# Performance work log

Measured on AMD Instinct MI355X. Metric: run time of the kernel, lower is better.

Reference implementation:

```python
import jax, jax.numpy as jnp
import numpy as np

G_NUM, K_DEG = 3, 3  # grid intervals, spline order (module defaults)
LN_EPS = 1e-5


def _bspline_basis(x, grid, k):
    """Cox-de Boor B-spline basis. x: [N, D], grid: [D, G+2k+1] -> [N, D, G+k]."""
    xg = x[:, :, None]                      # [N, D, 1]
    g = grid[None, :, :]                    # [1, D, M]
    B = ((xg >= g[..., :-1]) & (xg < g[..., 1:])).astype(x.dtype)  # degree 0
    for d in range(1, k + 1):
        left = (xg - g[..., :-(d + 1)]) / (g[..., d:-1] - g[..., :-(d + 1)])
        right = (g[..., d + 1:] - xg) / (g[..., d + 1:] - g[..., 1:-d])
        B = left * B[..., :-1] + right * B[..., 1:]
    return B                                # [N, D, G+k]


def _kan_layer(x, grid, coef, scale_base, scale_sp, node_scale, node_bias):
    # spline branch: fold per-edge scale_sp into coef, contract basis without
    # materializing the [N, in, out] per-edge tensor
    basis = _bspline_basis(x, grid, K_DEG)              # [N, in, G+k]
    coef_eff = coef * scale_sp[..., None]               # [in, out, G+k]
    y = jnp.einsum('nib,iob->no', basis, coef_eff)      # spline sum over edges
    y = y + jax.nn.silu(x) @ scale_base                 # residual base function
    return node_scale * y + node_bias                   # per-node affine


def setup_inputs() -> dict:
    key = jax.random.key(0)
    ks = jax.random.split(key, 12)
    B, S = 16, 1024
    D0, D1, D2 = 256, 512, 256
    nb = G_NUM + K_DEG  # num basis fns = 6
    h = 2.0 / G_NUM
    knots = np.arange(-K_DEG, G_NUM + K_DEG + 1) * h - 1.0  # [G+2k+1]=10, range [-3,3]
    grid1 = jnp.asarray(np.tile(knots, (D0, 1)), jnp.float32)
    grid2 = jnp.asarray(np.tile(knots, (D1, 1)), jnp.float32)
    inp = {
        'x': jax.random.normal(ks[0], (B, S, D0), jnp.float32),
        'grid1': grid1,
        'coef1': jax.random.normal(ks[1], (D0, D1, nb), jnp.float32) * 0.1,
        'scale_base1': jax.random.normal(ks[2], (D0, D1), jnp.float32) / np.sqrt(D0),
        'scale_sp1': jnp.ones((D0, D1), jnp.float32),
        'node_scale1': jnp.ones((D1,), jnp.float32),
        'node_bias1': jnp.zeros((D1,), jnp.float32),
        'grid2': grid2,
        'coef2': jax.random.normal(ks[3], (D1, D2, nb), jnp.float32) * 0.1,
        'scale_base2': jax.random.normal(ks[4], (D1, D2), jnp.float32) / np.sqrt(D1),
        'scale_sp2': jnp.ones((D1, D2), jnp.float32),
        'node_scale2': jnp.ones((D2,), jnp.float32),
        'node_bias2': jnp.zeros((D2,), jnp.float32),
        'ln_gamma': jnp.ones((D2,), jnp.float32),
        'ln_beta': jnp.zeros((D2,), jnp.float32),
    }
    return inp


def reference(x, grid1, coef1, scale_base1, scale_sp1, node_scale1, node_bias1,
              grid2, coef2, scale_base2, scale_sp2, node_scale2, node_bias2,
              ln_gamma, ln_beta):
    b, s, d = x.shape
    residual = x  # start_dim == final_dim -> residual path active
    h = x.reshape(-1, d)
    h = _kan_layer(h, grid1, coef1, scale_base1, scale_sp1, node_scale1, node_bias1)
    h = _kan_layer(h, grid2, coef2, scale_base2, scale_sp2, node_scale2, node_bias2)
    h = h.reshape(b, s, -1)
    h = h + residual
    # LayerNorm over last dim
    mu = jnp.mean(h, axis=-1, keepdims=True)
    var = jnp.mean((h - mu) ** 2, axis=-1, keepdims=True)
    h = (h - mu) * jax.lax.rsqrt(var + LN_EPS) * ln_gamma + ln_beta
    # torch nn.GELU default is exact (erf) variant
    return jax.nn.gelu(h, approximate=False)
```

## Files before the change

kernel.cpp:

```cpp
#include <hip/hip_runtime.h>
#include <cstdint>
#include <cstddef>

using f16   = _Float16;
using half8 = __attribute__((ext_vector_type(8))) _Float16;
using f32x4 = __attribute__((ext_vector_type(4))) float;
using ull   = unsigned long long;

#define DINL __device__ __forceinline__

DINL void gload_lds16(const void* gptr, void* lptr) {
  __builtin_amdgcn_global_load_lds(
      reinterpret_cast<const __attribute__((address_space(1))) uint32_t*>(
          reinterpret_cast<uintptr_t>(gptr)),
      reinterpret_cast<__attribute__((address_space(3))) uint32_t*>(
          reinterpret_cast<uintptr_t>(lptr)),
      16, 0, 0);
}

DINL unsigned pkh(float a, float b) {
  unsigned short ha = __builtin_bit_cast(unsigned short, (f16)a);
  unsigned short hb = __builtin_bit_cast(unsigned short, (f16)b);
  return (unsigned)ha | ((unsigned)hb << 16);
}

struct U4 { unsigned x, y, z, w; };

DINL U4 expand_pack(float x) {
  float xs = (x + 3.0f) * 1.5f;
  float mf = floorf(xs);
  int   m  = (int)mf;
  float u = xs - mf, u2 = u * u, u3 = u2 * u, um = 1.0f - u;
  float p3 = u3 * (1.0f / 6.0f);
  float p2 = (1.0f + 3.0f * (u + u2 - u3)) * (1.0f / 6.0f);
  float p1 = (4.0f - 6.0f * u2 + 3.0f * u3) * (1.0f / 6.0f);
  float p0 = um * um * um * (1.0f / 6.0f);
  ull P = (ull)pkh(p0, p1) | ((ull)pkh(p2, p3) << 32);
  if ((unsigned)m > 8u) P = 0;
  int s    = m * 16 - 48;
  int sneg = min(63, max(0, -s));
  int spos = min(63, max(0, s));
  int shi2 = min(63, max(0, s - 64));
  ull rlo = (s < 0) ? (P >> sneg) : ((s < 64) ? (P << spos) : 0ull);
  ull rhi = (s < 0) ? 0ull
                    : ((s < 64) ? ((P >> (63 - spos)) >> 1) : (P << shi2));
  float sil = x / (1.0f + __expf(-x));
  U4 r;
  r.x = (unsigned)rlo;
  r.y = (unsigned)(rlo >> 32);
  r.z = (unsigned)rhi;
  r.w = pkh(sil, 0.0f);
  return r;
}

__global__ __launch_bounds__(256)
void prep_w_kernel(const float* __restrict__ coef, const float* __restrict__ ssp,
                   const float* __restrict__ sb, f16* __restrict__ Wt,
                   int Din, int Dout) {
  int idx = blockIdx.x * 256 + threadIdx.x;
  if (idx >= Din * Dout) return;
  int n = idx / Din;
  int d = idx - n * Din;
  float s = ssp[(size_t)d * Dout + n];
  const float* c = coef + ((size_t)d * Dout + n) * 6;
  half8 wv;
#pragma unroll
  for (int b = 0; b < 6; ++b) wv[b] = (f16)(c[b] * s);
  wv[6] = (f16)sb[(size_t)d * Dout + n];
  wv[7] = (f16)0.0f;
  int dp = (d & ~7) | ((d & 7) ^ (n & 7));
  *reinterpret_cast<half8*>(Wt + ((size_t)n * Din + dp) * 8) = wv;
}

template <bool BIAS, int NS>
__global__ __launch_bounds__(512, 4)
void kan_gemm(const float* __restrict__ X, int ldx,
              const f16* __restrict__ Wt, int ldw,
              const float* __restrict__ nscale, const float* __restrict__ nbias,
              int N, float* __restrict__ Out) {
  __shared__ alignas(16) f16 A0[64 * 64];
  __shared__ alignas(16) f16 A1[64 * 64];
  __shared__ alignas(16) f16 B0[256 * 64];
  __shared__ alignas(16) f16 B1[256 * 64];

  const int tid  = threadIdx.x;
  const int w    = tid >> 6;
  const int lane = tid & 63;
  const int l15  = lane & 15, l7 = lane & 7, hi = lane >> 4;
  const int wm   = w >> 2, wn = w & 3;
  const int m0   = blockIdx.y * 64;
  const int n0   = blockIdx.x * 256;
  const int dim0 = blockIdx.z * (NS * 8);
  float* outz = Out + (size_t)blockIdx.z * ((size_t)gridDim.y * 64) * N;

  const int ar = tid >> 3, ad = tid & 7;
  const float* asrc = X + (size_t)(m0 + ar) * ldx + dim0 + ad;
  const int aoff = ar * 64 + 8 * (ad ^ (ar & 7));

  float xs[NS];
#pragma unroll
  for (int s = 0; s < NS; ++s) xs[s] = asrc[s * 8];

  const f16* wb[4];
  int ldsb[4];
#pragma unroll
  for (int q = 0; q < 4; ++q) {
    int c   = tid + q * 512;
    wb[q]   = Wt + (size_t)(n0 + (c >> 3)) * ldw + (size_t)dim0 * 8 + (c & 7) * 8;
    ldsb[q] = c * 8;
  }

  f32x4 acc[2][4] = {};

  auto stageB = [&](f16* buf, int k0) {
#pragma unroll
    for (int q = 0; q < 4; ++q) gload_lds16(wb[q] + k0, buf + ldsb[q]);
  };

  auto compute = [&](const f16* bA, const f16* bB) {
#pragma unroll
    for (int kk = 0; kk < 2; ++kk) {
      const int sl = kk * 4 + hi;
      half8 av[2], bv[4];
#pragma unroll
      for (int i = 0; i < 2; ++i)
        av[i] = *reinterpret_cast<const half8*>(
            bA + (wm * 32 + i * 16 + l15) * 64 + 8 * (sl ^ l7));
#pragma unroll
      for (int j = 0; j < 4; ++j)
        bv[j] = *reinterpret_cast<const half8*>(
            bB + (wn * 64 + j * 16 + l15) * 64 + 8 * (sl ^ l7));
#pragma unroll
      for (int i = 0; i < 2; ++i)
#pragma unroll
        for (int j = 0; j < 4; ++j)
          acc[i][j] = __builtin_amdgcn_mfma_f32_16x16x32_f16(av[i], bv[j], acc[i][j], 0, 0, 0);
    }
  };

  auto writeA = [&](f16* buf, U4 e) {
    *reinterpret_cast<U4*>(buf + aoff) = e;
  };

  stageB(B0, 0);
  writeA(A0, expand_pack(xs[0]));
  __syncthreads();

#pragma unroll
  for (int p = 0; p <= NS / 2 - 2; ++p) {
    stageB(B1, (2 * p + 1) * 64);
    compute(A0, B0);
    writeA(A1, expand_pack(xs[2 * p + 1]));
    __syncthreads();
    stageB(B0, (2 * p + 2) * 64);
    compute(A1, B1);
    writeA(A0, expand_pack(xs[2 * p + 2]));
    __syncthreads();
  }

  stageB(B1, (NS - 1) * 64);
  compute(A0, B0);
  writeA(A1, expand_pack(xs[NS - 1]));
  __syncthreads();
  compute(A1, B1);

#pragma unroll
  for (int j = 0; j < 4; ++j) {
    int col   = n0 + wn * 64 + j * 16 + l15;
    float nsv = nscale[col];
    float nbv = BIAS ? nbias[col] : 0.0f;
#pragma unroll
    for (int i = 0; i < 2; ++i) {
      int rb = m0 + wm * 32 + i * 16 + hi * 4;
#pragma unroll
      for (int r = 0; r < 4; ++r)
        outz[(size_t)(rb + r) * N + col] = nsv * acc[i][j][r] + nbv;
    }
  }
}

__global__ __launch_bounds__(256)
void ln_gelu_kernel(const float* __restrict__ P0, const float* __restrict__ P1,
                    const float* __restrict__ X,  const float* __restrict__ nb2,
                    const float* __restrict__ gamma, const float* __restrict__ beta,
                    float* __restrict__ out, int rows) {
  int row  = blockIdx.x * 4 + (threadIdx.x >> 6);
  int lane = threadIdx.x & 63;
  if (row >= rows) return;
  const float4 a  = *reinterpret_cast<const float4*>(P0 + (size_t)row * 256 + lane * 4);
  const float4 b  = *reinterpret_cast<const float4*>(P1 + (size_t)row * 256 + lane * 4);
  const float4 xr = *reinterpret_cast<const float4*>(X  + (size_t)row * 256 + lane * 4);
  const float4 nb = *reinterpret_cast<const float4*>(nb2 + lane * 4);
  const float4 g  = *reinterpret_cast<const float4*>(gamma + lane * 4);
  const float4 be = *reinterpret_cast<const float4*>(beta + lane * 4);
  float h[4] = { a.x + b.x + nb.x + xr.x, a.y + b.y + nb.y + xr.y,
                 a.z + b.z + nb.z + xr.z, a.w + b.w + nb.w + xr.w };
  float s = h[0] + h[1] + h[2] + h[3];
#pragma unroll
  for (int o = 32; o >= 1; o >>= 1) s += __shfl_xor(s, o);
  float mu = s * (1.0f / 256.0f);
  float vs = 0.f;
#pragma unroll
  for (int j = 0; j < 4; ++j) { float d = h[j] - mu; vs += d * d; }
#pragma unroll
  for (int o = 32; o >= 1; o >>= 1) vs += __shfl_xor(vs, o);
  float inv = rsqrtf(vs * (1.0f / 256.0f) + 1e-5f);
  float o4[4];
#pragma unroll
  for (int j = 0; j < 4; ++j) {
    float gj = (&g.x)[j], bj = (&be.x)[j];
    float v = (h[j] - mu) * inv * gj + bj;
    o4[j] = 0.5f * v * (1.0f + erff(v * 0.70710678118654752f));
  }
  *reinterpret_cast<float4*>(out + (size_t)row * 256 + lane * 4) =
      make_float4(o4[0], o4[1], o4[2], o4[3]);
}

extern "C" void kernel_launch(void* const* d_in, const int* in_sizes, int n_in,
                              void* d_out, int out_size, void* d_ws, size_t ws_size,
                              hipStream_t stream) {
  (void)in_sizes; (void)n_in; (void)out_size; (void)ws_size;
  const float* x     = (const float*)d_in[0];
  const float* coef1 = (const float*)d_in[2];
  const float* sb1   = (const float*)d_in[3];
  const float* ssp1  = (const float*)d_in[4];
  const float* ns1   = (const float*)d_in[5];
  const float* nb1   = (const float*)d_in[6];
  const float* coef2 = (const float*)d_in[8];
  const float* sb2   = (const float*)d_in[9];
  const float* ssp2  = (const float*)d_in[10];
  const float* ns2   = (const float*)d_in[11];
  const float* nb2   = (const float*)d_in[12];
  const float* lgam  = (const float*)d_in[13];
  const float* lbet  = (const float*)d_in[14];
  float* out = (float*)d_out;

  const int Ntok = 16 * 1024;
  const int D0 = 256, D1 = 512, D2 = 256;

  char*  ws   = (char*)d_ws;
  float* h1   = (float*)ws;
  size_t off  = (size_t)Ntok * D1 * sizeof(float);
  float* part = (float*)(ws + off);
  off += (size_t)2 * Ntok * D2 * sizeof(float);
  f16* Wt1 = (f16*)(ws + off);
  off += (size_t)D1 * D0 * 8 * sizeof(f16);
  f16* Wt2 = (f16*)(ws + off);

  prep_w_kernel<<<(D0 * D1 + 255) / 256, 256, 0, stream>>>(coef1, ssp1, sb1, Wt1, D0, D1);
  prep_w_kernel<<<(D1 * D2 + 255) / 256, 256, 0, stream>>>(coef2, ssp2, sb2, Wt2, D1, D2);

  kan_gemm<true, 32><<<dim3(D1 / 256, Ntok / 64, 1), 512, 0, stream>>>(
      x, D0, Wt1, D0 * 8, ns1, nb1, D1, h1);

  kan_gemm<false, 32><<<dim3(D2 / 256, Ntok / 64, 2), 512, 0, stream>>>(
      h1, D1, Wt2, D1 * 8, ns2, nullptr, D2, part);

  ln_gelu_kernel<<<Ntok / 4, 256, 0, stream>>>(
      part, part + (size_t)Ntok * D2, x, nb2, lgam, lbet, out, Ntok);
}
```

Before: 124.2 us.

## Retile KAN GEMM to 128x128 and expand spline basis directly into registers

Changes the block tile from 64x256 to 128x128 and gives each wave a 16-row strip that spans all 128 columns. Raw fp32 x values are now staged into LDS with async global-to-LDS loads and double-buffered alongside the weights. Each wave expands its own basis vectors in registers, so the A-operand LDS tile and its write are gone. The cost is that every lane evaluates the spline expansion twice per step, and the tile shape changes the balance of W and X reuse.

```diff
diff --git a/kernel.cpp b/kernel.cpp
--- a/kernel.cpp
+++ b/kernel.cpp
@@ -78,104 +78,93 @@
               const f16* __restrict__ Wt, int ldw,
               const float* __restrict__ nscale, const float* __restrict__ nbias,
               int N, float* __restrict__ Out) {
-  __shared__ alignas(16) f16 A0[64 * 64];
-  __shared__ alignas(16) f16 A1[64 * 64];
-  __shared__ alignas(16) f16 B0[256 * 64];
-  __shared__ alignas(16) f16 B1[256 * 64];
+  __shared__ alignas(16) f16   WB0[128 * 64];
+  __shared__ alignas(16) f16   WB1[128 * 64];
+  __shared__ alignas(16) float XB0[128 * 8];
+  __shared__ alignas(16) float XB1[128 * 8];
 
   const int tid  = threadIdx.x;
   const int w    = tid >> 6;
   const int lane = tid & 63;
   const int l15  = lane & 15, l7 = lane & 7, hi = lane >> 4;
-  const int wm   = w >> 2, wn = w & 3;
-  const int m0   = blockIdx.y * 64;
-  const int n0   = blockIdx.x * 256;
+  const int m0   = blockIdx.y * 128;
+  const int n0   = blockIdx.x * 128;
   const int dim0 = blockIdx.z * (NS * 8);
-  float* outz = Out + (size_t)blockIdx.z * ((size_t)gridDim.y * 64) * N;
-
-  const int ar = tid >> 3, ad = tid & 7;
-  const float* asrc = X + (size_t)(m0 + ar) * ldx + dim0 + ad;
-  const int aoff = ar * 64 + 8 * (ad ^ (ar & 7));
-
-  float xs[NS];
-#pragma unroll
-  for (int s = 0; s < NS; ++s) xs[s] = asrc[s * 8];
-
-  const f16* wb[4];
-  int ldsb[4];
-#pragma unroll
-  for (int q = 0; q < 4; ++q) {
-    int c   = tid + q * 512;
-    wb[q]   = Wt + (size_t)(n0 + (c >> 3)) * ldw + (size_t)dim0 * 8 + (c & 7) * 8;
-    ldsb[q] = c * 8;
-  }
-
-  f32x4 acc[2][4] = {};
-
-  auto stageB = [&](f16* buf, int k0) {
-#pragma unroll
-    for (int q = 0; q < 4; ++q) gload_lds16(wb[q] + k0, buf + ldsb[q]);
+  float* outz = Out + (size_t)blockIdx.z * ((size_t)gridDim.y * 128) * N;
+
+  const f16* wsrc0 = Wt + (size_t)(n0 + (tid >> 3)) * ldw + (size_t)dim0 * 8 + (tid & 7) * 8;
+  const f16* wsrc1 = Wt + (size_t)(n0 + ((tid + 512) >> 3)) * ldw + (size_t)dim0 * 8 + (tid & 7) * 8;
+  const int  wdst0 = tid * 8;
+  const int  wdst1 = (tid + 512) * 8;
+
+  const bool  xstager = (tid < 256);
+  const float* xsrc = X + (size_t)(m0 + (tid >> 1)) * ldx + dim0 + (tid & 1) * 4;
+  const int   xdst  = tid * 4;
+
+  const int xro = (w * 16 + l15) * 8 + hi;
+
+  f32x4 acc[8] = {};
+
+  auto stageW = [&](f16* buf, int ke) {
+    gload_lds16(wsrc0 + ke, buf + wdst0);
+    gload_lds16(wsrc1 + ke, buf + wdst1);
   };
-
-  auto compute = [&](const f16* bA, const f16* bB) {
-#pragma unroll
-    for (int kk = 0; kk < 2; ++kk) {
-      const int sl = kk * 4 + hi;
-      half8 av[2], bv[4];
-#pragma unroll
-      for (int i = 0; i < 2; ++i)
-        av[i] = *reinterpret_cast<const half8*>(
-            bA + (wm * 32 + i * 16 + l15) * 64 + 8 * (sl ^ l7));
-#pragma unroll
-      for (int j = 0; j < 4; ++j)
-        bv[j] = *reinterpret_cast<const half8*>(
-            bB + (wn * 64 + j * 16 + l15) * 64 + 8 * (sl ^ l7));
-#pragma unroll
-      for (int i = 0; i < 2; ++i)
-#pragma unroll
-        for (int j = 0; j < 4; ++j)
-          acc[i][j] = __builtin_amdgcn_mfma_f32_16x16x32_f16(av[i], bv[j], acc[i][j], 0, 0, 0);
+  auto stageX = [&](float* buf, int s) {
+    if (xstager) gload_lds16(xsrc + s * 8, buf + xdst);
+  };
+
+  auto step = [&](const float* xb, const f16* wb) {
+    float x0 = xb[xro];
+    float x1 = xb[xro + 4];
+    U4 e0 = expand_pack(x0);
+    U4 e1 = expand_pack(x1);
+    half8 a0 = __builtin_bit_cast(half8, e0);
+    half8 a1 = __builtin_bit_cast(half8, e1);
+#pragma unroll
+    for (int j = 0; j < 8; ++j) {
+      half8 bv = *reinterpret_cast<const half8*>(
+          wb + (j * 16 + l15) * 64 + 8 * (hi ^ l7));
+      acc[j] = __builtin_amdgcn_mfma_f32_16x16x32_f16(a0, bv, acc[j], 0, 0, 0);
+    }
+#pragma unroll
+    for (int j = 0; j < 8; ++j) {
+      half8 bv = *reinterpret_cast<const half8*>(
+          wb + (j * 16 + l15) * 64 + 8 * ((4 + hi) ^ l7));
+      acc[j] = __builtin_amdgcn_mfma_f32_16x16x32_f16(a1, bv, acc[j], 0, 0, 0);
     }
   };
 
-  auto writeA = [&](f16* buf, U4 e) {
-    *reinterpret_cast<U4*>(buf + aoff) = e;
-  };
-
-  stageB(B0, 0);
-  writeA(A0, expand_pack(xs[0]));
+  stageW(WB0, 0);
+  stageX(XB0, 0);
   __syncthreads();
 
-#pragma unroll
-  for (int p = 0; p <= NS / 2 - 2; ++p) {
-    stageB(B1, (2 * p + 1) * 64);
-    compute(A0, B0);
-    writeA(A1, expand_pack(xs[2 * p + 1]));
+  int ke = 64;
+  int sx = 1;
+  for (int p = 0; p < NS / 2 - 1; ++p) {
+    stageW(WB1, ke);       stageX(XB1, sx);
+    step(XB0, WB0);
     __syncthreads();
-    stageB(B0, (2 * p + 2) * 64);
-    compute(A1, B1);
-    writeA(A0, expand_pack(xs[2 * p + 2]));
+    stageW(WB0, ke + 64);  stageX(XB0, sx + 1);
+    step(XB1, WB1);
     __syncthreads();
+    ke += 128; sx += 2;
   }
 
-  stageB(B1, (NS - 1) * 64);
-  compute(A0, B0);
-  writeA(A1, expand_pack(xs[NS - 1]));
+  stageW(WB1, (NS - 1) * 64);
+  stageX(XB1, NS - 1);
+  step(XB0, WB0);
   __syncthreads();
-  compute(A1, B1);
-
-#pragma unroll
-  for (int j = 0; j < 4; ++j) {
-    int col   = n0 + wn * 64 + j * 16 + l15;
+  step(XB1, WB1);
+
+#pragma unroll
+  for (int j = 0; j < 8; ++j) {
+    int col   = n0 + j * 16 + l15;
     float nsv = nscale[col];
     float nbv = BIAS ? nbias[col] : 0.0f;
-#pragma unroll
-    for (int i = 0; i < 2; ++i) {
-      int rb = m0 + wm * 32 + i * 16 + hi * 4;
-#pragma unroll
-      for (int r = 0; r < 4; ++r)
-        outz[(size_t)(rb + r) * N + col] = nsv * acc[i][j][r] + nbv;
-    }
+    int rowb  = m0 + w * 16 + hi * 4;
+#pragma unroll
+    for (int r = 0; r < 4; ++r)
+      outz[(size_t)(rowb + r) * N + col] = nsv * acc[j][r] + nbv;
   }
 }
 
@@ -250,10 +239,10 @@
   prep_w_kernel<<<(D0 * D1 + 255) / 256, 256, 0, stream>>>(coef1, ssp1, sb1, Wt1, D0, D1);
   prep_w_kernel<<<(D1 * D2 + 255) / 256, 256, 0, stream>>>(coef2, ssp2, sb2, Wt2, D1, D2);
 
-  kan_gemm<true, 32><<<dim3(D1 / 256, Ntok / 64, 1), 512, 0, stream>>>(
+  kan_gemm<true, 32><<<dim3(D1 / 128, Ntok / 128, 1), 512, 0, stream>>>(
       x, D0, Wt1, D0 * 8, ns1, nb1, D1, h1);
 
-  kan_gemm<false, 32><<<dim3(D2 / 256, Ntok / 64, 2), 512, 0, stream>>>(
+  kan_gemm<false, 32><<<dim3(D2 / 128, Ntok / 128, 2), 512, 0, stream>>>(
       h1, D1, Wt2, D1 * 8, ns2, nullptr, D2, part);
 
   ln_gelu_kernel<<<Ntok / 4, 256, 0, stream>>>(
```

After: 139.8 us. +12.6%, slower.
